# Kernel tuning notes

Hardware: AMD Instinct MI355X
Metric: run time of the kernel (lower is better)

## Reference

```python
import jax, jax.numpy as jnp
import numpy as np

B, H, S, D = 2, 12, 4096, 768
BS = 64              # block size
HD = D // H          # head dim = 64
NB = S // BS         # 64 blocks
MC = 3               # max graph connections per block
PEN = -10000.0
RSQRT_D = 1.0 / np.sqrt(HD).astype(np.float32)


def setup_inputs() -> dict:
    key = jax.random.key(0)
    ks = jax.random.split(key, 6)
    hidden_states = jax.random.normal(ks[0], (B, S, D), jnp.float32)
    Wq = jax.random.normal(ks[1], (D, D), jnp.float32) * 0.02
    Wk = jax.random.normal(ks[2], (D, D), jnp.float32) * 0.02
    Wv = jax.random.normal(ks[3], (D, D), jnp.float32) * 0.02
    Wo = jax.random.normal(ks[4], (D, D), jnp.float32) * 0.02
    graph_attn = jax.random.randint(ks[5], (B, H, NB, MC), 0, NB, jnp.int32)
    return dict(
        hidden_states=hidden_states, Wq=Wq, Wk=Wk, Wv=Wv, Wo=Wo,
        band_mask=jnp.ones((B, 1, NB - 4, BS, 3 * BS), jnp.float32),
        from_mask=jnp.ones((B, 1, S, 1), jnp.float32),
        to_mask=jnp.ones((B, 1, 1, S), jnp.float32),
        from_blocked_mask=jnp.ones((B, NB, BS), jnp.float32),
        to_blocked_mask=jnp.ones((B, NB, BS), jnp.float32),
        graph_attn=graph_attn,
    )


def reference(hidden_states, Wq, Wk, Wv, Wo, band_mask, from_mask, to_mask,
              from_blocked_mask, to_blocked_mask, graph_attn):
    def proj(W):  # [B,S,D] -> [B,H,S,HD]
        return (hidden_states @ W.T).reshape(B, S, H, HD).transpose(0, 2, 1, 3)

    q, k, v = proj(Wq), proj(Wk), proj(Wv)
    bq = q.reshape(B, H, NB, BS, HD)
    bk = k.reshape(B, H, NB, BS, HD)
    bv = v.reshape(B, H, NB, BS, HD)

    # gather graph-selected key/value blocks: [B,H,NB,MC*BS,HD]
    gather = jax.vmap(jax.vmap(lambda blocks, idx: blocks[idx]))
    gk = gather(bk, graph_attn).reshape(B, H, NB, MC * BS, HD)
    gv = gather(bv, graph_attn).reshape(B, H, NB, MC * BS, HD)

    # graph mask from blocked masks: [B,H,NB,BS,MC*BS]
    gm = jax.vmap(lambda tm, ga: tm[ga])(to_blocked_mask, graph_attn)  # [B,H,NB,MC,BS]
    gm = gm.reshape(B, H, NB, MC * BS)
    graph_mask = jnp.einsum('blq,bhlk->bhlqk', from_blocked_mask, gm)

    # ---- first block: global attention over all keys ----
    fp = jnp.einsum('bhqd,bhkd->bhqk', bq[:, :, 0], k) * RSQRT_D + (1.0 - to_mask) * PEN
    first_ctx = jnp.einsum('bhqk,bhkd->bhqd', jax.nn.softmax(fp, -1), v)[:, :, None]

    # ---- second block: blocks 0,1,2,last + graph-gathered ----
    sk = jnp.concatenate([bk[:, :, 0], bk[:, :, 1], bk[:, :, 2], bk[:, :, -1], gk[:, :, 1]], axis=2)
    sv = jnp.concatenate([bv[:, :, 0], bv[:, :, 1], bv[:, :, 2], bv[:, :, -1], gv[:, :, 1]], axis=2)
    sp = jnp.einsum('bhqd,bhkd->bhqk', bq[:, :, 1], sk) * RSQRT_D
    seq_pad = jnp.concatenate([to_mask[:, :, :, :3 * BS], to_mask[:, :, :, -BS:],
                               jnp.ones((B, 1, 1, MC * BS), to_mask.dtype)], axis=3)
    rand_pad = jnp.concatenate([jnp.ones((B, H, BS, 4 * BS), graph_mask.dtype),
                                graph_mask[:, :, 1]], axis=3)
    sp = sp + (1.0 - jnp.minimum(seq_pad, rand_pad)) * PEN
    second_ctx = jnp.einsum('bhqk,bhkd->bhqd', jax.nn.softmax(sp, -1), sv)[:, :, None]

    # ---- middle blocks: sliding window (3 blocks) + first + last + graph ----
    ek = jnp.concatenate([bk[:, :, 1:-3], bk[:, :, 2:-2], bk[:, :, 3:-1]], axis=3)  # [B,H,NB-4,3BS,HD]
    ev = jnp.concatenate([bv[:, :, 1:-3], bv[:, :, 2:-2], bv[:, :, 3:-1]], axis=3)
    qm = bq[:, :, 2:-2]
    inner = jnp.einsum('bhlqd,bhlkd->bhlqk', qm, ek) * RSQRT_D + (1.0 - band_mask) * PEN
    randp = jnp.einsum('bhlqd,bhlkd->bhlqk', qm, gk[:, :, 2:-2]) * RSQRT_D + (1.0 - graph_mask[:, :, 2:-2]) * PEN
    firstp = jnp.einsum('bhlqd,bhkd->bhlqk', qm, bk[:, :, 0]) * RSQRT_D + (1.0 - to_mask[:, :, :, None, :BS]) * PEN
    lastp = jnp.einsum('bhlqd,bhkd->bhlqk', qm, bk[:, :, -1]) * RSQRT_D + (1.0 - to_mask[:, :, :, None, -BS:]) * PEN
    band = jnp.concatenate([firstp, inner, randp, lastp], axis=-1)
    attn = jax.nn.softmax(band, -1)
    mid_ctx = (jnp.einsum('bhlqk,bhlkd->bhlqd', attn[..., BS:4 * BS], ev)
               + jnp.einsum('bhlqk,bhlkd->bhlqd', attn[..., 4 * BS:4 * BS + MC * BS], gv[:, :, 2:-2])
               + jnp.einsum('bhlqk,bhkd->bhlqd', attn[..., :BS], bv[:, :, 0])
               + jnp.einsum('bhlqk,bhkd->bhlqd', attn[..., -BS:], bv[:, :, -1]))

    # ---- second-to-last block ----
    slk = jnp.concatenate([bk[:, :, 0], bk[:, :, -3], bk[:, :, -2], bk[:, :, -1], gk[:, :, -2]], axis=2)
    slv = jnp.concatenate([bv[:, :, 0], bv[:, :, -3], bv[:, :, -2], bv[:, :, -1], gv[:, :, -2]], axis=2)
    slp = jnp.einsum('bhqd,bhkd->bhqk', bq[:, :, -2], slk) * RSQRT_D
    sl_seq = jnp.concatenate([to_mask[:, :, :, :BS], to_mask[:, :, :, -3 * BS:],
                              jnp.ones((B, 1, 1, MC * BS), to_mask.dtype)], axis=3)
    sl_rand = jnp.concatenate([jnp.ones((B, H, BS, 4 * BS), graph_mask.dtype),
                               graph_mask[:, :, -2]], axis=3)
    slp = slp + (1.0 - jnp.minimum(sl_seq, sl_rand)) * PEN
    sl_ctx = jnp.einsum('bhqk,bhkd->bhqd', jax.nn.softmax(slp, -1), slv)[:, :, None]

    # ---- last block: global attention over all keys ----
    lp = jnp.einsum('bhqd,bhkd->bhqk', bq[:, :, -1], k) * RSQRT_D + (1.0 - to_mask) * PEN
    last_ctx = jnp.einsum('bhqk,bhkd->bhqd', jax.nn.softmax(lp, -1), v)[:, :, None]

    ctx = jnp.concatenate([first_ctx, second_ctx, mid_ctx, sl_ctx, last_ctx], axis=2)
    ctx = ctx.reshape(B, H, S, HD) * from_mask            # [B,H,S,HD]
    ctx = ctx.transpose(0, 2, 1, 3).reshape(B, S, D)      # [B,S,D]
    return ctx @ Wo.T                                     # output projection (no bias)
```

## Files before the change

### kernel.cpp

```cpp
#include <hip/hip_runtime.h>
#include <hip/hip_bf16.h>

#define BB 2
#define HH 12
#define SS 4096
#define DD 768
#define HD 64
#define NBK 64
#define MC 3

typedef __attribute__((ext_vector_type(8))) short short8_t;
typedef __attribute__((ext_vector_type(4))) float float4_t;

__device__ __forceinline__ unsigned short f2bf(float f) {
  union { float f; unsigned u; } c;
  c.f = f;
  unsigned u = c.u + 0x7FFFu + ((c.u >> 16) & 1u);
  return (unsigned short)(u >> 16);
}

__device__ __forceinline__ void gload16(const unsigned short* gp,
                                        unsigned short* lp) {
  __builtin_amdgcn_global_load_lds(
      (const __attribute__((address_space(1))) unsigned int*)gp,
      (__attribute__((address_space(3))) unsigned int*)lp, 16, 0, 0);
}

#define LDK 72

__global__ __launch_bounds__(256) void cvt_all(
    const float* __restrict__ hs, const float* __restrict__ Wq,
    const float* __restrict__ Wk, const float* __restrict__ Wv,
    const float* __restrict__ Wo, unsigned short* __restrict__ hsb,
    unsigned short* __restrict__ wqkvb, unsigned short* __restrict__ wob) {
  long i4 = (long)blockIdx.x * 256 + threadIdx.x;
  const float* src;
  unsigned short* dst;
  if (i4 < 1572864) {
    src = hs + i4 * 4;
    dst = hsb + i4 * 4;
  } else {
    long r = i4 - 1572864;
    int w = (int)(r / 147456);
    long e = r % 147456;
    src = (w == 0 ? Wq : w == 1 ? Wk : w == 2 ? Wv : Wo) + e * 4;
    dst = (w < 3) ? (wqkvb + (long)w * 589824 + e * 4) : (wob + e * 4);
  }
  float4_t v = *(const float4_t*)src;
  uint2 p;
  p.x = (unsigned)f2bf(v[0]) | ((unsigned)f2bf(v[1]) << 16);
  p.y = (unsigned)f2bf(v[2]) | ((unsigned)f2bf(v[3]) << 16);
  *(uint2*)dst = p;
}

#define STAGE_TILE(buf_, A_, B_, m0_, n0_, kt_)                               \
  {                                                                           \
    int rr_ = lane >> 3;                                                      \
    int cg_ = (lane & 7) ^ rr_;                                               \
    _Pragma("unroll") for (int u = 0; u < 4; u++) {                           \
      int g_ = w * 4 + u;                                                     \
      gload16(A_ + (size_t)(m0_ + g_ * 8 + rr_) * DD + kt_ + cg_ * 8,         \
              &As[buf_][g_ * 512]);                                           \
      gload16(B_ + (size_t)(n0_ + g_ * 8 + rr_) * DD + kt_ + cg_ * 8,         \
              &Bs[buf_][g_ * 512]);                                           \
    }                                                                         \
  }

#define LOAD_FRAGS(buf_, kk_)                                                 \
  int fr = lane & 15;                                                         \
  int qd = lane >> 4;                                                         \
  int cb = qd + ((kk_) >> 3);                                                 \
  short8_t af[4], bfr[4];                                                     \
  _Pragma("unroll") for (int i = 0; i < 4; i++) {                             \
    int r_ = wm + i * 16 + fr;                                                \
    af[i] = *(const short8_t*)&As[buf_][r_ * 64 + (cb ^ (fr & 7)) * 8];       \
  }                                                                           \
  _Pragma("unroll") for (int j = 0; j < 4; j++) {                             \
    int r_ = wn + j * 16 + fr;                                                \
    bfr[j] = *(const short8_t*)&Bs[buf_][r_ * 64 + (cb ^ (fr & 7)) * 8];      \
  }

__global__ __launch_bounds__(256) void gemm_qkv_b(
    const unsigned short* __restrict__ A, const unsigned short* __restrict__ W,
    unsigned short* __restrict__ qb, unsigned short* __restrict__ kb,
    unsigned short* __restrict__ vtb) {
  __shared__ unsigned short As[2][128 * 64];
  __shared__ unsigned short Bs[2][128 * 64];
  int tid = threadIdx.x;
  int m0 = blockIdx.x * 128;
  int n0 = blockIdx.y * 128;
  int lane = tid & 63;
  int w = tid >> 6;
  int wm = (w >> 1) * 64;
  int wn = (w & 1) * 64;
  int ysel = n0 / 768;

  float4_t acc[4][4];
#pragma unroll
  for (int i = 0; i < 4; i++)
#pragma unroll
    for (int j = 0; j < 4; j++)
#pragma unroll
      for (int r = 0; r < 4; r++) acc[i][j][r] = 0.f;

  STAGE_TILE(0, A, W, m0, n0, 0)
  int p = 0;

  if (ysel < 2) {
    for (int kt = 0; kt < DD; kt += 64) {
      __syncthreads();
      if (kt + 64 < DD) STAGE_TILE(p ^ 1, A, W, m0, n0, kt + 64)
#pragma unroll
      for (int kk = 0; kk < 64; kk += 32) {
        LOAD_FRAGS(p, kk)
#pragma unroll
        for (int i = 0; i < 4; i++)
#pragma unroll
          for (int j = 0; j < 4; j++)
            acc[j][i] = __builtin_amdgcn_mfma_f32_16x16x32_bf16(
                bfr[j], af[i], acc[j][i], 0, 0, 0);
      }
      p ^= 1;
    }
    int cn = lane & 15;
    int quad = lane >> 4;
    float scale = (ysel == 0) ? 0.125f : 1.0f;
    unsigned short* dst = (ysel == 0) ? qb : kb;
    int nb0 = n0 - ysel * 768;
#pragma unroll
    for (int j = 0; j < 4; j++)
#pragma unroll
      for (int i = 0; i < 4; i++) {
        int m = m0 + wm + i * 16 + cn;
        int nn = nb0 + wn + j * 16 + quad * 4;
        int b = m >> 12, s = m & 4095;
        int h = nn >> 6, d0 = nn & 63;
        uint2 pk;
        pk.x = (unsigned)f2bf(acc[j][i][0] * scale) |
               ((unsigned)f2bf(acc[j][i][1] * scale) << 16);
        pk.y = (unsigned)f2bf(acc[j][i][2] * scale) |
               ((unsigned)f2bf(acc[j][i][3] * scale) << 16);
        *(uint2*)&dst[(((size_t)b * HH + h) * SS + s) * HD + d0] = pk;
      }
  } else {
    for (int kt = 0; kt < DD; kt += 64) {
      __syncthreads();
      if (kt + 64 < DD) STAGE_TILE(p ^ 1, A, W, m0, n0, kt + 64)
#pragma unroll
      for (int kk = 0; kk < 64; kk += 32) {
        LOAD_FRAGS(p, kk)
#pragma unroll
        for (int i = 0; i < 4; i++)
#pragma unroll
          for (int j = 0; j < 4; j++)
            acc[i][j] = __builtin_amdgcn_mfma_f32_16x16x32_bf16(
                af[i], bfr[j], acc[i][j], 0, 0, 0);
      }
      p ^= 1;
    }
    int cn = lane & 15;
    int quad = lane >> 4;
    int nb0 = n0 - 1536;
#pragma unroll
    for (int i = 0; i < 4; i++)
#pragma unroll
      for (int j = 0; j < 4; j++) {
        int m = m0 + wm + i * 16 + quad * 4;
        int nn = nb0 + wn + j * 16 + cn;
        int b = m >> 12, s0 = m & 4095;
        int h = nn >> 6, d = nn & 63;
        uint2 pk;
        pk.x = (unsigned)f2bf(acc[i][j][0]) |
               ((unsigned)f2bf(acc[i][j][1]) << 16);
        pk.y = (unsigned)f2bf(acc[i][j][2]) |
               ((unsigned)f2bf(acc[i][j][3]) << 16);
        *(uint2*)&vtb[(((size_t)b * HH + h) * HD + d) * SS + s0] = pk;
      }
  }
}

__global__ __launch_bounds__(256) void gemm_out_b(
    const unsigned short* __restrict__ A, const unsigned short* __restrict__ W,
    float* __restrict__ dst) {
  __shared__ unsigned short As[2][128 * 64];
  __shared__ unsigned short Bs[2][128 * 64];
  int tid = threadIdx.x;
  int m0 = blockIdx.x * 128;
  int n0 = blockIdx.y * 128;
  int lane = tid & 63;
  int w = tid >> 6;
  int wm = (w >> 1) * 64;
  int wn = (w & 1) * 64;

  float4_t acc[4][4];
#pragma unroll
  for (int i = 0; i < 4; i++)
#pragma unroll
    for (int j = 0; j < 4; j++)
#pragma unroll
      for (int r = 0; r < 4; r++) acc[i][j][r] = 0.f;

  STAGE_TILE(0, A, W, m0, n0, 0)
  int p = 0;
  for (int kt = 0; kt < DD; kt += 64) {
    __syncthreads();
    if (kt + 64 < DD) STAGE_TILE(p ^ 1, A, W, m0, n0, kt + 64)
#pragma unroll
    for (int kk = 0; kk < 64; kk += 32) {
      LOAD_FRAGS(p, kk)
#pragma unroll
      for (int i = 0; i < 4; i++)
#pragma unroll
        for (int j = 0; j < 4; j++)
          acc[i][j] = __builtin_amdgcn_mfma_f32_16x16x32_bf16(
              af[i], bfr[j], acc[i][j], 0, 0, 0);
    }
    p ^= 1;
  }

  int cn = lane & 15;
  int rb = (lane >> 4) * 4;
#pragma unroll
  for (int i = 0; i < 4; i++)
#pragma unroll
    for (int j = 0; j < 4; j++)
#pragma unroll
      for (int r = 0; r < 4; r++) {
        int m = m0 + wm + i * 16 + rb + r;
        int n = n0 + wn + j * 16 + cn;
        dst[(size_t)m * DD + n] = acc[i][j][r];
      }
}

__global__ __launch_bounds__(256) void attn2(
    const unsigned short* __restrict__ q, const unsigned short* __restrict__ k,
    const unsigned short* __restrict__ vt, const int* __restrict__ graph,
    unsigned short* __restrict__ ctxb, float* __restrict__ part) {
  __shared__ unsigned short Ks[2][64 * LDK];
  __shared__ unsigned short Vs[2][64 * LDK];
  __shared__ unsigned short Ps[4][16 * LDK];

  int tid = threadIdx.x;
  int id = blockIdx.x;
  int b, h, l, nkb, heavy, chunk = 0, hid = 0;
  int list[8];
  if (id < 384) {
    heavy = 1;
    hid = id >> 3;
    chunk = id & 7;
    b = hid / 24;
    int r = hid % 24;
    h = r >> 1;
    l = (r & 1) ? (NBK - 1) : 0;
    nkb = 8;
#pragma unroll
    for (int i = 0; i < 8; i++) list[i] = chunk * 8 + i;
  } else {
    heavy = 0;
    int j = id - 384;
    b = j / 744;
    int r = j % 744;
    h = r / 62;
    l = 1 + r % 62;
    const int* g = graph + (((size_t)b * HH + h) * NBK + l) * MC;
    int n = 0;
    if (l == 1) {
      list[0] = 0; list[1] = 1; list[2] = 2; list[3] = NBK - 1; n = 4;
    } else if (l == NBK - 2) {
      list[0] = 0; list[1] = NBK - 3; list[2] = NBK - 2; list[3] = NBK - 1; n = 4;
    } else {
      list[0] = 0; list[1] = l - 1; list[2] = l; list[3] = l + 1;
      list[4] = NBK - 1; n = 5;
    }
    for (int m = 0; m < MC; m++) list[n++] = g[m];
    nkb = n;
  }
  size_t base = ((size_t)b * HH + h) * SS * HD;

  int lane = tid & 63;
  int w = tid >> 6;
  int lr = lane & 15;
  int quad = lane >> 4;

  short8_t qa[2];
  {
    const unsigned short* qp =
        q + base + (size_t)(l * 64 + w * 16 + lr) * HD + quad * 8;
    qa[0] = *(const short8_t*)qp;
    qa[1] = *(const short8_t*)(qp + 32);
  }

  float4_t Ot[4];
  float ls[4];
#pragma unroll
  for (int t = 0; t < 4; t++)
#pragma unroll
    for (int r = 0; r < 4; r++) Ot[t][r] = 0.f;
#pragma unroll
  for (int r = 0; r < 4; r++) ls[r] = 0.f;

  int srow = tid >> 3;
  int scol = (tid & 7) * 8;

  uint4 kr0, kr1, vr0, vr1;
  {
    int kb = list[0];
    const unsigned short* kp = k + base + (size_t)(kb * 64 + srow) * HD + scol;
    const unsigned short* vp = vt + base + (size_t)srow * SS + kb * 64 + scol;
    kr0 = *(const uint4*)kp;
    kr1 = *(const uint4*)(kp + 32 * HD);
    vr0 = *(const uint4*)vp;
    vr1 = *(const uint4*)(vp + 32 * SS);
  }
  *(uint4*)&Ks[0][srow * LDK + scol] = kr0;
  *(uint4*)&Ks[0][(srow + 32) * LDK + scol] = kr1;
  *(uint4*)&Vs[0][srow * LDK + scol] = vr0;
  *(uint4*)&Vs[0][(srow + 32) * LDK + scol] = vr1;
  int p = 0;

  for (int t = 0; t < nkb; t++) {
    __syncthreads();

    if (t + 1 < nkb) {
      int kb = list[t + 1];
      const unsigned short* kp = k + base + (size_t)(kb * 64 + srow) * HD + scol;
      const unsigned short* vp = vt + base + (size_t)srow * SS + kb * 64 + scol;
      kr0 = *(const uint4*)kp;
      kr1 = *(const uint4*)(kp + 32 * HD);
      vr0 = *(const uint4*)vp;
      vr1 = *(const uint4*)(vp + 32 * SS);
    }

    float4_t st[4];
#pragma unroll
    for (int tt = 0; tt < 4; tt++) {
#pragma unroll
      for (int r = 0; r < 4; r++) st[tt][r] = 0.f;
      short8_t kb0 = *(const short8_t*)&Ks[p][(tt * 16 + lr) * LDK + quad * 8];
      short8_t kb1 =
          *(const short8_t*)&Ks[p][(tt * 16 + lr) * LDK + quad * 8 + 32];
      st[tt] = __builtin_amdgcn_mfma_f32_16x16x32_bf16(qa[0], kb0, st[tt], 0, 0, 0);
      st[tt] = __builtin_amdgcn_mfma_f32_16x16x32_bf16(qa[1], kb1, st[tt], 0, 0, 0);
    }

#pragma unroll
    for (int tt = 0; tt < 4; tt++)
#pragma unroll
      for (int r = 0; r < 4; r++) {
        float pv = __expf(st[tt][r]);
        st[tt][r] = pv;
        ls[r] += pv;
        Ps[w][(quad * 4 + r) * LDK + tt * 16 + lr] = f2bf(pv);
      }

#pragma unroll
    for (int s = 0; s < 2; s++) {
      short8_t pa = *(const short8_t*)&Ps[w][lr * LDK + s * 32 + quad * 8];
#pragma unroll
      for (int tt = 0; tt < 4; tt++) {
        short8_t vb =
            *(const short8_t*)&Vs[p][(tt * 16 + lr) * LDK + s * 32 + quad * 8];
        Ot[tt] = __builtin_amdgcn_mfma_f32_16x16x32_bf16(pa, vb, Ot[tt], 0, 0, 0);
      }
    }

    if (t + 1 < nkb) {
      *(uint4*)&Ks[p ^ 1][srow * LDK + scol] = kr0;
      *(uint4*)&Ks[p ^ 1][(srow + 32) * LDK + scol] = kr1;
      *(uint4*)&Vs[p ^ 1][srow * LDK + scol] = vr0;
      *(uint4*)&Vs[p ^ 1][(srow + 32) * LDK + scol] = vr1;
    }
    p ^= 1;
  }

#pragma unroll
  for (int r = 0; r < 4; r++)
#pragma unroll
    for (int off = 1; off < 16; off <<= 1) ls[r] += __shfl_xor(ls[r], off);

  if (!heavy) {
#pragma unroll
    for (int r = 0; r < 4; r++) {
      float inv = 1.f / ls[r];
      size_t row = (size_t)b * SS + (size_t)l * 64 + w * 16 + quad * 4 + r;
#pragma unroll
      for (int tt = 0; tt < 4; tt++)
        ctxb[row * DD + h * HD + tt * 16 + lr] = f2bf(Ot[tt][r] * inv);
    }
  } else {
    float* pb = part + ((size_t)hid * 8 + chunk) * 4160;
#pragma unroll
    for (int r = 0; r < 4; r++) {
      int rowi = w * 16 + quad * 4 + r;
#pragma unroll
      for (int tt = 0; tt < 4; tt++)
        pb[rowi * 64 + tt * 16 + lr] = Ot[tt][r];
      if (lr == 0) pb[4096 + rowi] = ls[r];
    }
  }
}

__global__ __launch_bounds__(256) void reduce_heavy(
    const float* __restrict__ part, unsigned short* __restrict__ ctxb) {
  __shared__ float lrow[64];
  int hid = blockIdx.x;
  int tid = threadIdx.x;
  int b = hid / 24;
  int r = hid % 24;
  int h = r >> 1;
  int l = (r & 1) ? (NBK - 1) : 0;
  const float* pb = part + (size_t)hid * 8 * 4160;
  if (tid < 64) {
    float s = 0.f;
#pragma unroll
    for (int c = 0; c < 8; c++) s += pb[c * 4160 + 4096 + tid];
    lrow[tid] = s;
  }
  __syncthreads();
#pragma unroll
  for (int e = tid; e < 4096; e += 256) {
    float o = 0.f;
#pragma unroll
    for (int c = 0; c < 8; c++) o += pb[c * 4160 + e];
    int rowi = e >> 6, col = e & 63;
    size_t row = (size_t)b * SS + (size_t)l * 64 + rowi;
    ctxb[row * DD + h * HD + col] = f2bf(o / lrow[rowi]);
  }
}

extern "C" void kernel_launch(void* const* d_in, const int* in_sizes, int n_in,
                              void* d_out, int out_size, void* d_ws,
                              size_t ws_size, hipStream_t stream) {
  const float* hs = (const float*)d_in[0];
  const float* Wq = (const float*)d_in[1];
  const float* Wk = (const float*)d_in[2];
  const float* Wv = (const float*)d_in[3];
  const float* Wo = (const float*)d_in[4];
  const int* graph = (const int*)d_in[10];

  const size_t NHS = (size_t)BB * SS * DD;
  unsigned short* hsb = (unsigned short*)d_ws;
  unsigned short* wqkvb = hsb + NHS;
  unsigned short* wob = wqkvb + 3 * 768 * 768;
  unsigned short* qb = wob + 768 * 768;
  unsigned short* kb = qb + NHS;
  unsigned short* vtb = kb + NHS;
  unsigned short* ctxb = vtb + NHS;
  float* part = (float*)(ctxb + NHS);

  cvt_all<<<8448, 256, 0, stream>>>(hs, Wq, Wk, Wv, Wo, hsb, wqkvb, wob);
  gemm_qkv_b<<<dim3(64, 18, 1), 256, 0, stream>>>(hsb, wqkvb, qb, kb, vtb);
  attn2<<<1872, 256, 0, stream>>>(qb, kb, vtb, graph, ctxb, part);
  reduce_heavy<<<48, 256, 0, stream>>>(part, ctxb);
  gemm_out_b<<<dim3(64, 6, 1), 256, 0, stream>>>(ctxb, wob, (float*)d_out);
}
```

Before: 212.4 us.

## Rework projection GEMMs into 8-wave 256x128 tiles with triple-buffered split-phase pipeline

Both the QKV and output projection GEMMs now use 512-thread blocks with 256x128 output tiles instead of 256-thread 128x128 tiles. The K loop becomes a three-stage LDS ring: each iteration's global-to-LDS copies are split into two phases interleaved with the MFMA halves, and explicit vmcnt waits plus raw barriers and s_setprio replace __syncthreads. The goal is to hide global load latency behind the matrix multiplies and to raise operand reuse per block. In exchange it uses much more shared memory per block and halves the grid size, and the hand-written waitcnt and barrier schedule is fragile.

```diff
diff --git a/kernel.cpp b/kernel.cpp
--- a/kernel.cpp
+++ b/kernel.cpp
@@ -53,46 +53,118 @@
   *(uint2*)dst = p;
 }
 
-#define STAGE_TILE(buf_, A_, B_, m0_, n0_, kt_)                               \
-  {                                                                           \
-    int rr_ = lane >> 3;                                                      \
-    int cg_ = (lane & 7) ^ rr_;                                               \
-    _Pragma("unroll") for (int u = 0; u < 4; u++) {                           \
-      int g_ = w * 4 + u;                                                     \
-      gload16(A_ + (size_t)(m0_ + g_ * 8 + rr_) * DD + kt_ + cg_ * 8,         \
-              &As[buf_][g_ * 512]);                                           \
-      gload16(B_ + (size_t)(n0_ + g_ * 8 + rr_) * DD + kt_ + cg_ * 8,         \
-              &Bs[buf_][g_ * 512]);                                           \
-    }                                                                         \
-  }
-
-#define LOAD_FRAGS(buf_, kk_)                                                 \
-  int fr = lane & 15;                                                         \
-  int qd = lane >> 4;                                                         \
-  int cb = qd + ((kk_) >> 3);                                                 \
-  short8_t af[4], bfr[4];                                                     \
-  _Pragma("unroll") for (int i = 0; i < 4; i++) {                             \
-    int r_ = wm + i * 16 + fr;                                                \
-    af[i] = *(const short8_t*)&As[buf_][r_ * 64 + (cb ^ (fr & 7)) * 8];       \
-  }                                                                           \
-  _Pragma("unroll") for (int j = 0; j < 4; j++) {                             \
-    int r_ = wn + j * 16 + fr;                                                \
-    bfr[j] = *(const short8_t*)&Bs[buf_][r_ * 64 + (cb ^ (fr & 7)) * 8];      \
-  }
-
-__global__ __launch_bounds__(256) void gemm_qkv_b(
+#define BARX()                       \
+  do {                               \
+    asm volatile("" ::: "memory");   \
+    __builtin_amdgcn_s_barrier();    \
+    asm volatile("" ::: "memory");   \
+  } while (0)
+#define VMW(n) asm volatile("s_waitcnt vmcnt(" #n ")" ::: "memory")
+
+#define ST_PH0(s_, kt_)                                                   \
+  {                                                                       \
+    gload16(Ag + (kt_), &As[s_][rr * 64 + ch * 8]);                       \
+    gload16(Ag + (kt_) + 64 * DD, &As[s_][(64 + rr) * 64 + ch * 8]);      \
+    gload16(Bg + (kt_), &Bs[s_][rr * 64 + ch * 8]);                       \
+  }
+#define ST_PH1(s_, kt_)                                                   \
+  {                                                                       \
+    gload16(Ag + (kt_) + 128 * DD, &As[s_][(128 + rr) * 64 + ch * 8]);    \
+    gload16(Ag + (kt_) + 192 * DD, &As[s_][(192 + rr) * 64 + ch * 8]);    \
+    gload16(Bg + (kt_) + 64 * DD, &Bs[s_][(64 + rr) * 64 + ch * 8]);      \
+  }
+
+#define LDA8(kx)                                                          \
+  _Pragma("unroll") for (int i = 0; i < 4; i++) {                         \
+    int r_ = wm + i * 16 + fr;                                            \
+    af[kx][i] = *(const short8_t*)&As[sl][r_ * 64 +                       \
+                                          (((kx)*4 + qd) ^ (r_ & 7)) * 8]; \
+  }
+#define LDB4(j0)                                                          \
+  _Pragma("unroll") for (int jj = 0; jj < 2; jj++) {                      \
+    int r_ = wn + ((j0) + jj) * 16 + fr;                                  \
+    bf[0][jj] =                                                           \
+        *(const short8_t*)&Bs[sl][r_ * 64 + ((qd) ^ (r_ & 7)) * 8];       \
+    bf[1][jj] =                                                           \
+        *(const short8_t*)&Bs[sl][r_ * 64 + ((4 + qd) ^ (r_ & 7)) * 8];   \
+  }
+
+#define KLOOP(MM0, MM1)                                                   \
+  ST_PH0(0, 0) ST_PH1(0, 0)                         \
+  ST_PH0(1, 64) ST_PH1(1, 64)                       \
+  VMW(6);                  \
+  BARX();                                                                 \
+  int sl = 0;                                                             \
+  for (int T = 0; T < 12; ++T) {                                          \
+    int s2 = sl + 2;                                                      \
+    if (s2 >= 3) s2 -= 3;                                                 \
+    int ktn = (T + 2) * 64;                                               \
+    short8_t af[2][4], bf[2][2];                                          \
+                             \
+    LDA8(0) LDA8(1) LDB4(0)                                               \
+    if (T <= 9) ST_PH0(s2, ktn)                                           \
+    BARX();                                                               \
+    __builtin_amdgcn_s_setprio(1);                                        \
+    _Pragma("unroll") for (int jj = 0; jj < 2; jj++)                      \
+        _Pragma("unroll") for (int i = 0; i < 4; i++) { MM0(jj, i) }      \
+    __builtin_amdgcn_s_setprio(0);                                        \
+    BARX();                                                               \
+                   \
+    LDB4(2)                                                               \
+    if (T <= 9) ST_PH1(s2, ktn)                                           \
+    BARX();                                                               \
+    __builtin_amdgcn_s_setprio(1);                                        \
+    _Pragma("unroll") for (int jj = 0; jj < 2; jj++)                      \
+        _Pragma("unroll") for (int i = 0; i < 4; i++) { MM1(jj, i) }      \
+    __builtin_amdgcn_s_setprio(0);                                        \
+    if (T < 11) {                                                         \
+      if (T <= 9) { VMW(6); } else { VMW(0); }                            \
+      BARX();                                                             \
+    }                                                                     \
+    sl = (sl == 2) ? 0 : sl + 1;                                          \
+  }
+
+#define MFQK0(jj, i)                                                      \
+  acc[jj][i] = __builtin_amdgcn_mfma_f32_16x16x32_bf16(                   \
+      bf[0][jj], af[0][i], acc[jj][i], 0, 0, 0);                          \
+  acc[jj][i] = __builtin_amdgcn_mfma_f32_16x16x32_bf16(                   \
+      bf[1][jj], af[1][i], acc[jj][i], 0, 0, 0);
+#define MFQK1(jj, i)                                                      \
+  acc[(jj) + 2][i] = __builtin_amdgcn_mfma_f32_16x16x32_bf16(             \
+      bf[0][jj], af[0][i], acc[(jj) + 2][i], 0, 0, 0);                    \
+  acc[(jj) + 2][i] = __builtin_amdgcn_mfma_f32_16x16x32_bf16(             \
+      bf[1][jj], af[1][i], acc[(jj) + 2][i], 0, 0, 0);
+#define MFN0(jj, i)                                                       \
+  acc[i][jj] = __builtin_amdgcn_mfma_f32_16x16x32_bf16(                   \
+      af[0][i], bf[0][jj], acc[i][jj], 0, 0, 0);                          \
+  acc[i][jj] = __builtin_amdgcn_mfma_f32_16x16x32_bf16(                   \
+      af[1][i], bf[1][jj], acc[i][jj], 0, 0, 0);
+#define MFN1(jj, i)                                                       \
+  acc[i][(jj) + 2] = __builtin_amdgcn_mfma_f32_16x16x32_bf16(             \
+      af[0][i], bf[0][jj], acc[i][(jj) + 2], 0, 0, 0);                    \
+  acc[i][(jj) + 2] = __builtin_amdgcn_mfma_f32_16x16x32_bf16(             \
+      af[1][i], bf[1][jj], acc[i][(jj) + 2], 0, 0, 0);
+
+__global__ __launch_bounds__(512, 2) void gemm_qkv8(
     const unsigned short* __restrict__ A, const unsigned short* __restrict__ W,
     unsigned short* __restrict__ qb, unsigned short* __restrict__ kb,
     unsigned short* __restrict__ vtb) {
-  __shared__ unsigned short As[2][128 * 64];
-  __shared__ unsigned short Bs[2][128 * 64];
+  __shared__ unsigned short As[3][256 * 64];
+  __shared__ unsigned short Bs[3][128 * 64];
   int tid = threadIdx.x;
-  int m0 = blockIdx.x * 128;
+  int m0 = blockIdx.x * 256;
   int n0 = blockIdx.y * 128;
   int lane = tid & 63;
   int w = tid >> 6;
   int wm = (w >> 1) * 64;
   int wn = (w & 1) * 64;
+  int fr = lane & 15;
+  int qd = lane >> 4;
+  int rr = tid >> 3;
+  int ch = tid & 7;
+  int cg = ch ^ (rr & 7);
+  const unsigned short* Ag = A + (size_t)(m0 + rr) * DD + cg * 8;
+  const unsigned short* Bg = W + (size_t)(n0 + rr) * DD + cg * 8;
   int ysel = n0 / 768;
 
   float4_t acc[4][4];
@@ -103,27 +175,8 @@
 #pragma unroll
       for (int r = 0; r < 4; r++) acc[i][j][r] = 0.f;
 
-  STAGE_TILE(0, A, W, m0, n0, 0)
-  int p = 0;
-
   if (ysel < 2) {
-    for (int kt = 0; kt < DD; kt += 64) {
-      __syncthreads();
-      if (kt + 64 < DD) STAGE_TILE(p ^ 1, A, W, m0, n0, kt + 64)
-#pragma unroll
-      for (int kk = 0; kk < 64; kk += 32) {
-        LOAD_FRAGS(p, kk)
-#pragma unroll
-        for (int i = 0; i < 4; i++)
-#pragma unroll
-          for (int j = 0; j < 4; j++)
-            acc[j][i] = __builtin_amdgcn_mfma_f32_16x16x32_bf16(
-                bfr[j], af[i], acc[j][i], 0, 0, 0);
-      }
-      p ^= 1;
-    }
-    int cn = lane & 15;
-    int quad = lane >> 4;
+    KLOOP(MFQK0, MFQK1)
     float scale = (ysel == 0) ? 0.125f : 1.0f;
     unsigned short* dst = (ysel == 0) ? qb : kb;
     int nb0 = n0 - ysel * 768;
@@ -131,8 +184,8 @@
     for (int j = 0; j < 4; j++)
 #pragma unroll
       for (int i = 0; i < 4; i++) {
-        int m = m0 + wm + i * 16 + cn;
-        int nn = nb0 + wn + j * 16 + quad * 4;
+        int m = m0 + wm + i * 16 + fr;
+        int nn = nb0 + wn + j * 16 + qd * 4;
         int b = m >> 12, s = m & 4095;
         int h = nn >> 6, d0 = nn & 63;
         uint2 pk;
@@ -143,30 +196,14 @@
         *(uint2*)&dst[(((size_t)b * HH + h) * SS + s) * HD + d0] = pk;
       }
   } else {
-    for (int kt = 0; kt < DD; kt += 64) {
-      __syncthreads();
-      if (kt + 64 < DD) STAGE_TILE(p ^ 1, A, W, m0, n0, kt + 64)
-#pragma unroll
-      for (int kk = 0; kk < 64; kk += 32) {
-        LOAD_FRAGS(p, kk)
-#pragma unroll
-        for (int i = 0; i < 4; i++)
-#pragma unroll
-          for (int j = 0; j < 4; j++)
-            acc[i][j] = __builtin_amdgcn_mfma_f32_16x16x32_bf16(
-                af[i], bfr[j], acc[i][j], 0, 0, 0);
-      }
-      p ^= 1;
-    }
-    int cn = lane & 15;
-    int quad = lane >> 4;
+    KLOOP(MFN0, MFN1)
     int nb0 = n0 - 1536;
 #pragma unroll
     for (int i = 0; i < 4; i++)
 #pragma unroll
       for (int j = 0; j < 4; j++) {
-        int m = m0 + wm + i * 16 + quad * 4;
-        int nn = nb0 + wn + j * 16 + cn;
+        int m = m0 + wm + i * 16 + qd * 4;
+        int nn = nb0 + wn + j * 16 + fr;
         int b = m >> 12, s0 = m & 4095;
         int h = nn >> 6, d = nn & 63;
         uint2 pk;
@@ -179,18 +216,25 @@
   }
 }
 
-__global__ __launch_bounds__(256) void gemm_out_b(
+__global__ __launch_bounds__(512, 2) void gemm_out8(
     const unsigned short* __restrict__ A, const unsigned short* __restrict__ W,
     float* __restrict__ dst) {
-  __shared__ unsigned short As[2][128 * 64];
-  __shared__ unsigned short Bs[2][128 * 64];
+  __shared__ unsigned short As[3][256 * 64];
+  __shared__ unsigned short Bs[3][128 * 64];
   int tid = threadIdx.x;
-  int m0 = blockIdx.x * 128;
+  int m0 = blockIdx.x * 256;
   int n0 = blockIdx.y * 128;
   int lane = tid & 63;
   int w = tid >> 6;
   int wm = (w >> 1) * 64;
   int wn = (w & 1) * 64;
+  int fr = lane & 15;
+  int qd = lane >> 4;
+  int rr = tid >> 3;
+  int ch = tid & 7;
+  int cg = ch ^ (rr & 7);
+  const unsigned short* Ag = A + (size_t)(m0 + rr) * DD + cg * 8;
+  const unsigned short* Bg = W + (size_t)(n0 + rr) * DD + cg * 8;
 
   float4_t acc[4][4];
 #pragma unroll
@@ -200,26 +244,9 @@
 #pragma unroll
       for (int r = 0; r < 4; r++) acc[i][j][r] = 0.f;
 
-  STAGE_TILE(0, A, W, m0, n0, 0)
-  int p = 0;
-  for (int kt = 0; kt < DD; kt += 64) {
-    __syncthreads();
-    if (kt + 64 < DD) STAGE_TILE(p ^ 1, A, W, m0, n0, kt + 64)
-#pragma unroll
-    for (int kk = 0; kk < 64; kk += 32) {
-      LOAD_FRAGS(p, kk)
-#pragma unroll
-      for (int i = 0; i < 4; i++)
-#pragma unroll
-        for (int j = 0; j < 4; j++)
-          acc[i][j] = __builtin_amdgcn_mfma_f32_16x16x32_bf16(
-              af[i], bfr[j], acc[i][j], 0, 0, 0);
-    }
-    p ^= 1;
-  }
-
-  int cn = lane & 15;
-  int rb = (lane >> 4) * 4;
+  KLOOP(MFN0, MFN1)
+
+  int rb = qd * 4;
 #pragma unroll
   for (int i = 0; i < 4; i++)
 #pragma unroll
@@ -227,7 +254,7 @@
 #pragma unroll
       for (int r = 0; r < 4; r++) {
         int m = m0 + wm + i * 16 + rb + r;
-        int n = n0 + wn + j * 16 + cn;
+        int n = n0 + wn + j * 16 + fr;
         dst[(size_t)m * DD + n] = acc[i][j][r];
       }
 }
@@ -449,8 +476,8 @@
   float* part = (float*)(ctxb + NHS);
 
   cvt_all<<<8448, 256, 0, stream>>>(hs, Wq, Wk, Wv, Wo, hsb, wqkvb, wob);
-  gemm_qkv_b<<<dim3(64, 18, 1), 256, 0, stream>>>(hsb, wqkvb, qb, kb, vtb);
+  gemm_qkv8<<<dim3(32, 18, 1), 512, 0, stream>>>(hsb, wqkvb, qb, kb, vtb);
   attn2<<<1872, 256, 0, stream>>>(qb, kb, vtb, graph, ctxb, part);
   reduce_heavy<<<48, 256, 0, stream>>>(part, ctxb);
-  gemm_out_b<<<dim3(64, 6, 1), 256, 0, stream>>>(ctxb, wob, (float*)d_out);
-}
+  gemm_out8<<<dim3(32, 6, 1), 512, 0, stream>>>(ctxb, wob, (float*)d_out);
+}
```

Result: slower. 218.0 us (+2.6%).

## Load GEMM weight fragments directly from global memory instead of LDS

Applied to the files above, without the earlier changes.

Both projection GEMMs stop staging the weight (B) tile through shared memory; each wave now reads its B fragments straight from global memory with 16-byte loads, and only the activation tile is double-buffered in LDS. This halves LDS use per block and the async-copy traffic, and launch bounds now request 4 blocks per CU to gain occupancy. The cost is that the global loads now sit on the MFMA critical path without prefetch, and each weight element is fetched by both M-row waves, relying on cache hits.

```diff
diff --git a/kernel.cpp b/kernel.cpp
--- a/kernel.cpp
+++ b/kernel.cpp
@@ -53,7 +53,7 @@
   *(uint2*)dst = p;
 }
 
-#define STAGE_TILE(buf_, A_, B_, m0_, n0_, kt_)                               \
+#define STAGE_A(buf_, A_, m0_, kt_)                                           \
   {                                                                           \
     int rr_ = lane >> 3;                                                      \
     int cg_ = (lane & 7) ^ rr_;                                               \
@@ -61,31 +61,24 @@
       int g_ = w * 4 + u;                                                     \
       gload16(A_ + (size_t)(m0_ + g_ * 8 + rr_) * DD + kt_ + cg_ * 8,         \
               &As[buf_][g_ * 512]);                                           \
-      gload16(B_ + (size_t)(n0_ + g_ * 8 + rr_) * DD + kt_ + cg_ * 8,         \
-              &Bs[buf_][g_ * 512]);                                           \
     }                                                                         \
   }
 
-#define LOAD_FRAGS(buf_, kk_)                                                 \
-  int fr = lane & 15;                                                         \
-  int qd = lane >> 4;                                                         \
+#define LOAD_FRAGS_AB(buf_, kt_, kk_)                                         \
   int cb = qd + ((kk_) >> 3);                                                 \
   short8_t af[4], bfr[4];                                                     \
   _Pragma("unroll") for (int i = 0; i < 4; i++) {                             \
     int r_ = wm + i * 16 + fr;                                                \
     af[i] = *(const short8_t*)&As[buf_][r_ * 64 + (cb ^ (fr & 7)) * 8];       \
   }                                                                           \
-  _Pragma("unroll") for (int j = 0; j < 4; j++) {                             \
-    int r_ = wn + j * 16 + fr;                                                \
-    bfr[j] = *(const short8_t*)&Bs[buf_][r_ * 64 + (cb ^ (fr & 7)) * 8];      \
-  }
-
-__global__ __launch_bounds__(256) void gemm_qkv_b(
+  _Pragma("unroll") for (int j = 0; j < 4; j++)                               \
+    bfr[j] = *(const short8_t*)&Wg[(size_t)(j * 16) * DD + (kt_) + (kk_)];
+
+__global__ __launch_bounds__(256, 4) void gemm_qkv_b(
     const unsigned short* __restrict__ A, const unsigned short* __restrict__ W,
     unsigned short* __restrict__ qb, unsigned short* __restrict__ kb,
     unsigned short* __restrict__ vtb) {
   __shared__ unsigned short As[2][128 * 64];
-  __shared__ unsigned short Bs[2][128 * 64];
   int tid = threadIdx.x;
   int m0 = blockIdx.x * 128;
   int n0 = blockIdx.y * 128;
@@ -93,7 +86,10 @@
   int w = tid >> 6;
   int wm = (w >> 1) * 64;
   int wn = (w & 1) * 64;
+  int fr = lane & 15;
+  int qd = lane >> 4;
   int ysel = n0 / 768;
+  const unsigned short* Wg = W + (size_t)(n0 + wn + fr) * DD + qd * 8;
 
   float4_t acc[4][4];
 #pragma unroll
@@ -103,16 +99,16 @@
 #pragma unroll
       for (int r = 0; r < 4; r++) acc[i][j][r] = 0.f;
 
-  STAGE_TILE(0, A, W, m0, n0, 0)
+  STAGE_A(0, A, m0, 0)
   int p = 0;
 
   if (ysel < 2) {
     for (int kt = 0; kt < DD; kt += 64) {
       __syncthreads();
-      if (kt + 64 < DD) STAGE_TILE(p ^ 1, A, W, m0, n0, kt + 64)
+      if (kt + 64 < DD) STAGE_A(p ^ 1, A, m0, kt + 64)
 #pragma unroll
       for (int kk = 0; kk < 64; kk += 32) {
-        LOAD_FRAGS(p, kk)
+        LOAD_FRAGS_AB(p, kt, kk)
 #pragma unroll
         for (int i = 0; i < 4; i++)
 #pragma unroll
@@ -145,10 +141,10 @@
   } else {
     for (int kt = 0; kt < DD; kt += 64) {
       __syncthreads();
-      if (kt + 64 < DD) STAGE_TILE(p ^ 1, A, W, m0, n0, kt + 64)
+      if (kt + 64 < DD) STAGE_A(p ^ 1, A, m0, kt + 64)
 #pragma unroll
       for (int kk = 0; kk < 64; kk += 32) {
-        LOAD_FRAGS(p, kk)
+        LOAD_FRAGS_AB(p, kt, kk)
 #pragma unroll
         for (int i = 0; i < 4; i++)
 #pragma unroll
@@ -179,11 +175,10 @@
   }
 }
 
-__global__ __launch_bounds__(256) void gemm_out_b(
+__global__ __launch_bounds__(256, 4) void gemm_out_b(
     const unsigned short* __restrict__ A, const unsigned short* __restrict__ W,
     float* __restrict__ dst) {
   __shared__ unsigned short As[2][128 * 64];
-  __shared__ unsigned short Bs[2][128 * 64];
   int tid = threadIdx.x;
   int m0 = blockIdx.x * 128;
   int n0 = blockIdx.y * 128;
@@ -191,6 +186,9 @@
   int w = tid >> 6;
   int wm = (w >> 1) * 64;
   int wn = (w & 1) * 64;
+  int fr = lane & 15;
+  int qd = lane >> 4;
+  const unsigned short* Wg = W + (size_t)(n0 + wn + fr) * DD + qd * 8;
 
   float4_t acc[4][4];
 #pragma unroll
@@ -200,14 +198,14 @@
 #pragma unroll
       for (int r = 0; r < 4; r++) acc[i][j][r] = 0.f;
 
-  STAGE_TILE(0, A, W, m0, n0, 0)
+  STAGE_A(0, A, m0, 0)
   int p = 0;
   for (int kt = 0; kt < DD; kt += 64) {
     __syncthreads();
-    if (kt + 64 < DD) STAGE_TILE(p ^ 1, A, W, m0, n0, kt + 64)
+    if (kt + 64 < DD) STAGE_A(p ^ 1, A, m0, kt + 64)
 #pragma unroll
     for (int kk = 0; kk < 64; kk += 32) {
-      LOAD_FRAGS(p, kk)
+      LOAD_FRAGS_AB(p, kt, kk)
 #pragma unroll
       for (int i = 0; i < 4; i++)
 #pragma unroll
```

Measured after the change: 260.4 us. 1.23x slower.
